# Performance work log

Measured on AMD Instinct MI355X. Metric: run time of the kernel, lower is better.

The kernel has to match this reference:

```python
import jax, jax.numpy as jnp
import numpy as np


def _class_stats(x, labels, C):
    # x: [N, D] float scores; labels: [N] int class ids in [0, C)
    N, D = x.shape
    ones = jnp.ones((N,), x.dtype)
    counts = jax.ops.segment_sum(ones, labels, num_segments=C)                 # [C]
    sums = jax.ops.segment_sum(x, labels, num_segments=C)                      # [C, D]
    safe = jnp.maximum(counts, 1.0)
    means = sums / safe[:, None]                                               # per-class mean, [C, D]
    total = sums.sum(axis=0)                                                   # [D]
    other = (total[None, :] - sums) / jnp.maximum(N - counts, 1.0)[:, None]    # complement mean, [C, D]
    # intra-class L1 spread: mean over (count_c * D) elements per class
    intra_row = jnp.abs(x - means[labels]).sum(axis=-1)                        # [N]
    intra = jax.ops.segment_sum(intra_row, labels, num_segments=C) / (safe * D)
    diff = jnp.exp(-5.0 * jnp.abs(means - other).mean(axis=-1))                # [C]
    present = counts > 0
    n_present = present.sum()
    # original: if only one unique class, diff term is exp(0) == 1
    diff = jnp.where(n_present > 1, diff, jnp.ones_like(diff))
    return intra, diff, present


def setup_inputs() -> dict:
    key = jax.random.key(0)
    k1, k2 = jax.random.split(key)
    N, C = 2_000_000, 32
    pred = jax.random.normal(k1, (N, C), dtype=jnp.float32)
    pseudo = jax.random.normal(k2, (N, C), dtype=jnp.float32)
    return {"pred": pred, "pseudo": pseudo}


def reference(pred, pseudo):
    # used_labels=False branch of LossClassInOut
    C = pred.shape[-1]
    pseudo_labels = jnp.argmax(pseudo, axis=-1)
    pred_labels = jnp.argmax(pred, axis=-1)
    # pred stats segmented by pseudo labels; pseudo stats segmented by pred labels
    pred_loss, pred_diff, pres_a = _class_stats(pred, pseudo_labels, C)
    pseudo_loss, pseudo_diff, pres_b = _class_stats(pseudo, pred_labels, C)
    pa = pres_a.astype(pred.dtype)
    pb = pres_b.astype(pred.dtype)
    num = (pred_loss * pa).sum() + (pred_diff * pa).sum() + (pseudo_loss * pb).sum() + (pseudo_diff * pb).sum()
    den = 2.0 * pa.sum() + 2.0 * pb.sum()
    return num / den
```

## Files before the change

kernel.cpp:

```cpp
#include <hip/hip_runtime.h>


constexpr int CDIM = 32;
constexpr int NBLK = 512;
constexpr int ROWS_PER_BLOCK = 128;

typedef __attribute__((ext_vector_type(8)))  short bf16x8;
typedef __attribute__((ext_vector_type(16))) float f32x16;

__device__ __forceinline__ unsigned short f2bf(float f) {
    unsigned u = __float_as_uint(f);
    return (unsigned short)((u + 0x7FFFu + ((u >> 16) & 1u)) >> 16);
}
__device__ __forceinline__ int toff(int r, int kb) {
    return r * 32 + ((kb ^ (r & 7)) * 4);
}
__device__ __forceinline__ void argmax16(const float4* v, float& bv, int& bi) {
    float b = v[0].x; int i = 0;
#pragma unroll
    for (int k = 0; k < 4; k++) {
        int k4 = k * 4;
        if (v[k].x > b) { b = v[k].x; i = k4; }
        if (v[k].y > b) { b = v[k].y; i = k4 + 1; }
        if (v[k].z > b) { b = v[k].z; i = k4 + 2; }
        if (v[k].w > b) { b = v[k].w; i = k4 + 3; }
    }
    bv = b; bi = i;
}
__device__ __forceinline__ int combine_argmax(float bv, int bc, int h2) {
    float ov = __shfl_xor(bv, 32);
    int   oc = __shfl_xor(bc, 32);
    float vlo = h2 ? ov : bv, vhi = h2 ? bv : ov;
    int   clo = h2 ? oc : bc, chi = h2 ? bc : oc;
    return (vhi > vlo) ? chi : clo;
}

__device__ __forceinline__ void stage_tile(const float4* __restrict__ g4,
                                           float* lds, long long wb,
                                           int nrows, int lw)
{
    const int rl = lw >> 3;
    const int kb = (lw & 7) ^ (rl & 7);
#pragma unroll
    for (int i = 0; i < 4; i++) {
        long long r = wb + 8 * i + rl; if (r >= nrows) r = nrows - 1;
        __builtin_amdgcn_global_load_lds(
            (const __attribute__((address_space(1))) void*)(g4 + r * 8 + kb),
            (__attribute__((address_space(3))) void*)(lds + i * 256),
            16, 0, 0);
    }
}

__global__ __launch_bounds__(256) void pass1_kernel(
    const float* __restrict__ pred, const float* __restrict__ pseudo,
    float* __restrict__ ws, int nrows)
{
    __shared__ __align__(16) float ptile[4][2][32 * 32];
    __shared__ __align__(16) float qtile[4][2][32 * 32];
    __shared__ __align__(16) unsigned short labs[4][32];
    __shared__ float sa[CDIM][33], sb[CDIM][33];
    __shared__ float ca[CDIM], cb[CDIM];

    const int t = threadIdx.x, wv = t >> 6, lw = t & 63;
    for (int i = t; i < CDIM * 33; i += 256) { (&sa[0][0])[i] = 0.f; (&sb[0][0])[i] = 0.f; }
    if (t < CDIM) { ca[t] = 0.f; cb[t] = 0.f; }
    __syncthreads();

    const int n = lw & 31, h2 = lw >> 5;

    f32x16 accP, accQ;
#pragma unroll
    for (int g = 0; g < 16; g++) { accP[g] = 0.f; accQ[g] = 0.f; }

    const float4* p4 = (const float4*)pred;
    const float4* q4 = (const float4*)pseudo;
    const long long rps = (long long)NBLK * ROWS_PER_BLOCK;
    const int nsweep = (int)((nrows + rps - 1) / rps);
    const long long wbase0 = (long long)blockIdx.x * ROWS_PER_BLOCK + wv * 32;

    stage_tile(p4, ptile[wv][0], wbase0, nrows, lw);
    stage_tile(q4, qtile[wv][0], wbase0, nrows, lw);

    for (int s = 0; s < nsweep; s++) {
        const long long wb = wbase0 + (long long)s * rps;
        const int cur = s & 1;
        if (s + 1 < nsweep) {
            const long long wb2 = wb + rps;
            stage_tile(p4, ptile[wv][cur ^ 1], wb2, nrows, lw);
            stage_tile(q4, qtile[wv][cur ^ 1], wb2, nrows, lw);
            asm volatile("s_waitcnt vmcnt(8)" ::: "memory");
        } else {
            asm volatile("s_waitcnt vmcnt(0)" ::: "memory");
        }
        __builtin_amdgcn_sched_barrier(0);
        float* pt = ptile[wv][cur];
        float* qt = qtile[wv][cur];

        const int r = n;
        const bool valid = (wb + r) < nrows;
        int la, lbv;
        {
            float4 v_[4];
#pragma unroll
            for (int k = 0; k < 4; k++) v_[k] = *(const float4*)&qt[toff(r, 4 * h2 + k)];
            float bv; int bi; argmax16(v_, bv, bi);
            la = combine_argmax(bv, 16 * h2 + bi, h2);
#pragma unroll
            for (int k = 0; k < 4; k++) v_[k] = *(const float4*)&pt[toff(r, 4 * h2 + k)];
            argmax16(v_, bv, bi);
            lbv = combine_argmax(bv, 16 * h2 + bi, h2);
        }
        if (h2 == 0) {
            labs[wv][r] = (unsigned short)((valid ? la : 0xFF) | ((valid ? lbv : 0xFF) << 8));
            unsafeAtomicAdd(&ca[la & 31], valid ? 1.f : 0.f);
            unsafeAtomicAdd(&cb[lbv & 31], valid ? 1.f : 0.f);
        }

#pragma unroll
        for (int kt = 0; kt < 2; kt++) {
            const uint4 lv = *(const uint4*)&labs[wv][kt * 16 + h2 * 8];
            bf16x8 aP, aQ, bP, bQ;
#pragma unroll
            for (int j = 0; j < 8; j++) {
                unsigned w32 = ((const unsigned*)&lv)[j >> 1];
                unsigned pr  = (w32 >> ((j & 1) * 16)) & 0xFFFFu;
                int laj = (int)(pr & 0xFF), lbj = (int)(pr >> 8);
                aP[j] = (short)((laj == n) ? 0x3F80 : 0);
                aQ[j] = (short)((lbj == n) ? 0x3F80 : 0);
                int rr = kt * 16 + h2 * 8 + j;
                int o = rr * 32 + (((n >> 2) ^ (rr & 7)) * 4) + (n & 3);
                bP[j] = (short)f2bf(pt[o]);
                bQ[j] = (short)f2bf(qt[o]);
            }
            accP = __builtin_amdgcn_mfma_f32_32x32x16_bf16(aP, bP, accP, 0, 0, 0);
            accQ = __builtin_amdgcn_mfma_f32_32x32x16_bf16(aQ, bQ, accQ, 0, 0, 0);
        }
    }

#pragma unroll
    for (int g = 0; g < 16; g++) {
        int c = (g & 3) + 8 * (g >> 2) + 4 * h2;
        unsafeAtomicAdd(&sa[c][n], accP[g]);
        unsafeAtomicAdd(&sb[c][n], accQ[g]);
    }
    __syncthreads();
    for (int i = t; i < CDIM * CDIM; i += 256) {
        int c = i >> 5, d = i & 31;
        unsafeAtomicAdd(&ws[64 + i],        sa[c][d]);
        unsafeAtomicAdd(&ws[64 + 1024 + i], sb[c][d]);
    }
    if (t < CDIM) { unsafeAtomicAdd(&ws[t], ca[t]); unsafeAtomicAdd(&ws[32 + t], cb[t]); }
}

__global__ __launch_bounds__(256) void pass2_kernel(
    const float* __restrict__ pred, const float* __restrict__ pseudo,
    float* __restrict__ ws, int nrows)
{
    __shared__ __align__(16) float ptile[4][2][32 * 32];
    __shared__ __align__(16) float qtile[4][2][32 * 32];
    __shared__ __align__(16) float mA[1024], mB[1024];
    __shared__ float ia[CDIM], ib[CDIM];

    const int t = threadIdx.x, wv = t >> 6, lw = t & 63;
    for (int i = t; i < 1024; i += 256) {
        int c = i >> 5, d = i & 31;
        int o = c * 32 + (((d >> 2) ^ (c & 7)) * 4) + (d & 3);
        mA[o] = ws[64 + i]        / fmaxf(ws[c],      1.f);
        mB[o] = ws[64 + 1024 + i] / fmaxf(ws[32 + c], 1.f);
    }
    if (t < CDIM) { ia[t] = 0.f; ib[t] = 0.f; }
    __syncthreads();

    const int n = lw & 31, h2 = lw >> 5;

    const float4* p4 = (const float4*)pred;
    const float4* q4 = (const float4*)pseudo;
    const long long rps = (long long)NBLK * ROWS_PER_BLOCK;
    const int nsweep = (int)((nrows + rps - 1) / rps);
    const long long wbase0 = (long long)blockIdx.x * ROWS_PER_BLOCK + wv * 32;

    stage_tile(p4, ptile[wv][0], wbase0, nrows, lw);
    stage_tile(q4, qtile[wv][0], wbase0, nrows, lw);

    for (int s = 0; s < nsweep; s++) {
        const long long wb = wbase0 + (long long)s * rps;
        const int cur = s & 1;
        if (s + 1 < nsweep) {
            const long long wb2 = wb + rps;
            stage_tile(p4, ptile[wv][cur ^ 1], wb2, nrows, lw);
            stage_tile(q4, qtile[wv][cur ^ 1], wb2, nrows, lw);
            asm volatile("s_waitcnt vmcnt(8)" ::: "memory");
        } else {
            asm volatile("s_waitcnt vmcnt(0)" ::: "memory");
        }
        __builtin_amdgcn_sched_barrier(0);
        float* pt = ptile[wv][cur];
        float* qt = qtile[wv][cur];

        const int r = n;
        const bool valid = (wb + r) < nrows;
        float4 pr_[4], qr_[4];
#pragma unroll
        for (int k = 0; k < 4; k++) { pr_[k] = *(const float4*)&pt[toff(r, 4 * h2 + k)];
                                      qr_[k] = *(const float4*)&qt[toff(r, 4 * h2 + k)]; }
        float bv; int bi;
        argmax16(qr_, bv, bi);
        const int la = combine_argmax(bv, 16 * h2 + bi, h2) & 31;
        argmax16(pr_, bv, bi);
        const int lb = combine_argmax(bv, 16 * h2 + bi, h2) & 31;

        float sA = 0.f, sB = 0.f;
#pragma unroll
        for (int k = 0; k < 4; k++) {
            float4 m4 = *(const float4*)&mA[la * 32 + (((4 * h2 + k) ^ (la & 7)) * 4)];
            sA += fabsf(pr_[k].x - m4.x) + fabsf(pr_[k].y - m4.y)
                + fabsf(pr_[k].z - m4.z) + fabsf(pr_[k].w - m4.w);
            float4 n4 = *(const float4*)&mB[lb * 32 + (((4 * h2 + k) ^ (lb & 7)) * 4)];
            sB += fabsf(qr_[k].x - n4.x) + fabsf(qr_[k].y - n4.y)
                + fabsf(qr_[k].z - n4.z) + fabsf(qr_[k].w - n4.w);
        }
        unsafeAtomicAdd(&ia[la], valid ? sA : 0.f);
        unsafeAtomicAdd(&ib[lb], valid ? sB : 0.f);
    }
    __syncthreads();
    if (t < CDIM) {
        unsafeAtomicAdd(&ws[2112 + t], ia[t]);
        unsafeAtomicAdd(&ws[2144 + t], ib[t]);
    }
}

__global__ __launch_bounds__(64) void finalize_kernel(
    const float* __restrict__ ws, float* __restrict__ out, int nrows)
{
    __shared__ float tota[CDIM];
    __shared__ float totb[CDIM];
    int t = threadIdx.x;
    if (t < CDIM) {
        float sa_ = 0.f, sb_ = 0.f;
        for (int c = 0; c < CDIM; c++) {
            sa_ += ws[64 + c * 32 + t];
            sb_ += ws[64 + 1024 + c * 32 + t];
        }
        tota[t] = sa_; totb[t] = sb_;
    }
    __syncthreads();

    const int  c   = t & 31;
    const bool isA = (t < 32);
    const float* sums = isA ? (ws + 64) : (ws + 64 + 1024);
    const float* tot  = isA ? tota : totb;
    float cnt  = isA ? ws[c]        : ws[32 + c];
    float isum = isA ? ws[2112 + c] : ws[2144 + c];

    float safe = fmaxf(cnt, 1.0f);
    float invs = 1.0f / safe;
    float invo = 1.0f / fmaxf((float)nrows - cnt, 1.0f);
    float mad = 0.f;
    for (int d = 0; d < CDIM; d++) {
        float s = sums[c * 32 + d];
        float m = s * invs;
        float o = (tot[d] - s) * invo;
        mad += fabsf(m - o);
    }
    mad *= (1.0f / CDIM);
    float diff = expf(-5.0f * mad);
    float present = (cnt > 0.f) ? 1.f : 0.f;

    unsigned long long pm = __ballot(cnt > 0.f);
    int np = isA ? __popcll(pm & 0xFFFFFFFFull) : __popcll(pm >> 32);
    if (np <= 1) diff = 1.0f;

    float intra   = isum * invs * (1.0f / CDIM);
    float contrib = present * (intra + diff);
    float pres    = present;
#pragma unroll
    for (int m = 1; m < 64; m <<= 1) {
        contrib += __shfl_xor(contrib, m, 64);
        pres    += __shfl_xor(pres,    m, 64);
    }
    if (t == 0) out[0] = contrib / (2.0f * pres);
}

extern "C" void kernel_launch(void* const* d_in, const int* in_sizes, int n_in,
                              void* d_out, int out_size, void* d_ws, size_t ws_size,
                              hipStream_t stream) {
    const float* pred   = (const float*)d_in[0];
    const float* pseudo = (const float*)d_in[1];
    float* ws  = (float*)d_ws;
    float* out = (float*)d_out;
    const int nrows = in_sizes[0] / CDIM;

    hipMemsetAsync(d_ws, 0, 2176 * sizeof(float), stream);

    dim3 grid(NBLK), block(256);
    pass1_kernel<<<grid, block, 0, stream>>>(pred, pseudo, ws, nrows);
    pass2_kernel<<<grid, block, 0, stream>>>(pred, pseudo, ws, nrows);
    finalize_kernel<<<1, 64, 0, stream>>>(ws, out, nrows);
}
```

Before: 601.0 us.

## Replace LDS double-buffer async loads with register prefetch and raise occupancy

Swaps the direct global-to-LDS double-buffered staging for register-staged prefetch: the next tile is loaded into registers while the current single-buffered LDS tile is processed, then written to LDS. Halving the tile LDS footprint and adding launch bounds with a minimum of 3 blocks per CU lets more blocks reside, and the grid grows from 512 to 768 blocks. It aims to raise memory parallelism through occupancy. The cost is extra VGPR pressure, an LDS write pass, and a full vmcnt(0) wait each iteration.

```diff
diff --git a/kernel.cpp b/kernel.cpp
--- a/kernel.cpp
+++ b/kernel.cpp
@@ -2,7 +2,7 @@
 
 
 constexpr int CDIM = 32;
-constexpr int NBLK = 512;
+constexpr int NBLK = 768;
 constexpr int ROWS_PER_BLOCK = 128;
 
 typedef __attribute__((ext_vector_type(8)))  short bf16x8;
@@ -35,28 +35,30 @@
     return (vhi > vlo) ? chi : clo;
 }
 
-__device__ __forceinline__ void stage_tile(const float4* __restrict__ g4,
-                                           float* lds, long long wb,
-                                           int nrows, int lw)
+__device__ __forceinline__ void load_tile_regs(const float4* __restrict__ g4,
+                                               float4* R, long long wb,
+                                               int nrows, int lw)
 {
     const int rl = lw >> 3;
     const int kb = (lw & 7) ^ (rl & 7);
 #pragma unroll
     for (int i = 0; i < 4; i++) {
         long long r = wb + 8 * i + rl; if (r >= nrows) r = nrows - 1;
-        __builtin_amdgcn_global_load_lds(
-            (const __attribute__((address_space(1))) void*)(g4 + r * 8 + kb),
-            (__attribute__((address_space(3))) void*)(lds + i * 256),
-            16, 0, 0);
-    }
-}
-
-__global__ __launch_bounds__(256) void pass1_kernel(
+        R[i] = g4[r * 8 + kb];
+    }
+}
+__device__ __forceinline__ void write_tile(float* lds, const float4* R, int lw) {
+#pragma unroll
+    for (int i = 0; i < 4; i++)
+        *(float4*)&lds[i * 256 + lw * 4] = R[i];
+}
+
+__global__ __launch_bounds__(256, 3) void pass1_kernel(
     const float* __restrict__ pred, const float* __restrict__ pseudo,
     float* __restrict__ ws, int nrows)
 {
-    __shared__ __align__(16) float ptile[4][2][32 * 32];
-    __shared__ __align__(16) float qtile[4][2][32 * 32];
+    __shared__ __align__(16) float ptile[4][32 * 32];
+    __shared__ __align__(16) float qtile[4][32 * 32];
     __shared__ __align__(16) unsigned short labs[4][32];
     __shared__ float sa[CDIM][33], sb[CDIM][33];
     __shared__ float ca[CDIM], cb[CDIM];
@@ -78,23 +80,23 @@
     const int nsweep = (int)((nrows + rps - 1) / rps);
     const long long wbase0 = (long long)blockIdx.x * ROWS_PER_BLOCK + wv * 32;
 
-    stage_tile(p4, ptile[wv][0], wbase0, nrows, lw);
-    stage_tile(q4, qtile[wv][0], wbase0, nrows, lw);
+    float* pt = ptile[wv];
+    float* qt = qtile[wv];
+
+    float4 P[4], Q[4];
+    load_tile_regs(p4, P, wbase0, nrows, lw);
+    load_tile_regs(q4, Q, wbase0, nrows, lw);
+    asm volatile("s_waitcnt vmcnt(0)" ::: "memory");
+    write_tile(pt, P, lw);
+    write_tile(qt, Q, lw);
 
     for (int s = 0; s < nsweep; s++) {
         const long long wb = wbase0 + (long long)s * rps;
-        const int cur = s & 1;
-        if (s + 1 < nsweep) {
-            const long long wb2 = wb + rps;
-            stage_tile(p4, ptile[wv][cur ^ 1], wb2, nrows, lw);
-            stage_tile(q4, qtile[wv][cur ^ 1], wb2, nrows, lw);
-            asm volatile("s_waitcnt vmcnt(8)" ::: "memory");
-        } else {
-            asm volatile("s_waitcnt vmcnt(0)" ::: "memory");
-        }
-        __builtin_amdgcn_sched_barrier(0);
-        float* pt = ptile[wv][cur];
-        float* qt = qtile[wv][cur];
+        const bool pf = (s + 1 < nsweep);
+        if (pf) {
+            load_tile_regs(p4, P, wb + rps, nrows, lw);
+            load_tile_regs(q4, Q, wb + rps, nrows, lw);
+        }
 
         const int r = n;
         const bool valid = (wb + r) < nrows;
@@ -135,6 +137,13 @@
             accP = __builtin_amdgcn_mfma_f32_32x32x16_bf16(aP, bP, accP, 0, 0, 0);
             accQ = __builtin_amdgcn_mfma_f32_32x32x16_bf16(aQ, bQ, accQ, 0, 0, 0);
         }
+
+        if (pf) {
+            asm volatile("s_waitcnt vmcnt(0)" ::: "memory");
+            __builtin_amdgcn_sched_barrier(0);
+            write_tile(pt, P, lw);
+            write_tile(qt, Q, lw);
+        }
     }
 
 #pragma unroll
@@ -152,12 +161,12 @@
     if (t < CDIM) { unsafeAtomicAdd(&ws[t], ca[t]); unsafeAtomicAdd(&ws[32 + t], cb[t]); }
 }
 
-__global__ __launch_bounds__(256) void pass2_kernel(
+__global__ __launch_bounds__(256, 3) void pass2_kernel(
     const float* __restrict__ pred, const float* __restrict__ pseudo,
     float* __restrict__ ws, int nrows)
 {
-    __shared__ __align__(16) float ptile[4][2][32 * 32];
-    __shared__ __align__(16) float qtile[4][2][32 * 32];
+    __shared__ __align__(16) float ptile[4][32 * 32];
+    __shared__ __align__(16) float qtile[4][32 * 32];
     __shared__ __align__(16) float mA[1024], mB[1024];
     __shared__ float ia[CDIM], ib[CDIM];
 
@@ -179,23 +188,23 @@
     const int nsweep = (int)((nrows + rps - 1) / rps);
     const long long wbase0 = (long long)blockIdx.x * ROWS_PER_BLOCK + wv * 32;
 
-    stage_tile(p4, ptile[wv][0], wbase0, nrows, lw);
-    stage_tile(q4, qtile[wv][0], wbase0, nrows, lw);
+    float* pt = ptile[wv];
+    float* qt = qtile[wv];
+
+    float4 P[4], Q[4];
+    load_tile_regs(p4, P, wbase0, nrows, lw);
+    load_tile_regs(q4, Q, wbase0, nrows, lw);
+    asm volatile("s_waitcnt vmcnt(0)" ::: "memory");
+    write_tile(pt, P, lw);
+    write_tile(qt, Q, lw);
 
     for (int s = 0; s < nsweep; s++) {
         const long long wb = wbase0 + (long long)s * rps;
-        const int cur = s & 1;
-        if (s + 1 < nsweep) {
-            const long long wb2 = wb + rps;
-            stage_tile(p4, ptile[wv][cur ^ 1], wb2, nrows, lw);
-            stage_tile(q4, qtile[wv][cur ^ 1], wb2, nrows, lw);
-            asm volatile("s_waitcnt vmcnt(8)" ::: "memory");
-        } else {
-            asm volatile("s_waitcnt vmcnt(0)" ::: "memory");
-        }
-        __builtin_amdgcn_sched_barrier(0);
-        float* pt = ptile[wv][cur];
-        float* qt = qtile[wv][cur];
+        const bool pf = (s + 1 < nsweep);
+        if (pf) {
+            load_tile_regs(p4, P, wb + rps, nrows, lw);
+            load_tile_regs(q4, Q, wb + rps, nrows, lw);
+        }
 
         const int r = n;
         const bool valid = (wb + r) < nrows;
@@ -221,6 +230,13 @@
         }
         unsafeAtomicAdd(&ia[la], valid ? sA : 0.f);
         unsafeAtomicAdd(&ib[lb], valid ? sB : 0.f);
+
+        if (pf) {
+            asm volatile("s_waitcnt vmcnt(0)" ::: "memory");
+            __builtin_amdgcn_sched_barrier(0);
+            write_tile(pt, P, lw);
+            write_tile(qt, Q, lw);
+        }
     }
     __syncthreads();
     if (t < CDIM) {
```

Measured after the change: 783.7 us. 30.4% more time.
